# Performance work log

Measured on AMD Instinct MI355X. Metric: run time of the kernel, lower is better.

Reference implementation:

```python
import jax, jax.numpy as jnp
import numpy as np
import math

D_MODEL = 2048
NUM_HEADS = 16
HEAD_DIM = D_MODEL // NUM_HEADS
B, QLEN, CACHE_LEN = 4, 512, 3584

def setup_inputs() -> dict:
    key = jax.random.key(0)
    ks = jax.random.split(key, 13)
    s = 0.02
    return {
        'query': jax.random.normal(ks[0], (B, QLEN, D_MODEL), jnp.float32),
        'key': jax.random.normal(ks[1], (B, QLEN, D_MODEL), jnp.float32),
        'value': jax.random.normal(ks[2], (B, QLEN, D_MODEL), jnp.float32),
        'cached_k': jax.random.normal(ks[3], (B, CACHE_LEN, D_MODEL), jnp.float32),
        'cached_v': jax.random.normal(ks[4], (B, CACHE_LEN, D_MODEL), jnp.float32),
        'wq': jax.random.normal(ks[5], (D_MODEL, D_MODEL), jnp.float32) * s,
        'bq': jnp.zeros((D_MODEL,), jnp.float32),
        'wk': jax.random.normal(ks[6], (D_MODEL, D_MODEL), jnp.float32) * s,
        'bk': jnp.zeros((D_MODEL,), jnp.float32),
        'wv': jax.random.normal(ks[7], (D_MODEL, D_MODEL), jnp.float32) * s,
        'bv': jnp.zeros((D_MODEL,), jnp.float32),
        'wo': jax.random.normal(ks[8], (D_MODEL, D_MODEL), jnp.float32) * s,
        'bo': jnp.zeros((D_MODEL,), jnp.float32),
    }

def _split_heads(x):
    b, s, _ = x.shape
    return x.reshape(b, s, NUM_HEADS, HEAD_DIM).transpose(0, 2, 1, 3)  # [b,h,s,d]

def reference(query, key, value, cached_k, cached_v, wq, bq, wk, bk, wv, bv, wo, bo):
    # projections (torch Linear: x @ W^T + b)
    Q = query @ wq.T + bq
    K_new = key @ wk.T + bk
    V_new = value @ wv.T + bv
    K = jnp.concatenate([cached_k, K_new], axis=1)  # [b, total, d_model]
    V = jnp.concatenate([cached_v, V_new], axis=1)
    seq_len = query.shape[1]
    total_len = K.shape[1]
    cache_len = total_len - seq_len
    Qh = _split_heads(Q)  # [b,h,q,d]
    Kh = _split_heads(K)  # [b,h,t,d]
    Vh = _split_heads(V)
    scale = math.sqrt(HEAD_DIM)
    scores = jnp.einsum('bhqd,bhtd->bhqt', Qh, Kh) / scale
    # causal mask with cache offset: query i attends to keys j <= cache_len + i
    q_idx = jnp.arange(seq_len)[:, None]
    k_idx = jnp.arange(total_len)[None, :]
    mask = k_idx > (q_idx + cache_len)  # True = masked
    scores = jnp.where(mask[None, None], -jnp.inf, scores)
    attn = jax.nn.softmax(scores, axis=-1)
    out = jnp.einsum('bhqt,bhtd->bhqd', attn, Vh)
    out = out.transpose(0, 2, 1, 3).reshape(query.shape[0], seq_len, D_MODEL)
    out = out @ wo.T + bo
    return out
```

## Files before the change

kernel.cpp:

```cpp
#include <hip/hip_runtime.h>

typedef _Float16 half8 __attribute__((ext_vector_type(8)));
typedef _Float16 half4v __attribute__((ext_vector_type(4)));
typedef float f32x4 __attribute__((ext_vector_type(4)));

#define NB 4
#define SQ 512
#define CL 3584
#define TT 4096
#define DM 2048
#define NH 16
#define DH 128

#define KSW(row, col) ((((row) * 128) + (col)) ^ ((((row) & 7) << 3)))
#define VSW(row, col) ((((row) * 64) + (col)) ^ ((((row) & 7) << 3)))
#define PSW(row, col) ((((row) * 64) + (col)) ^ ((((row) & 7) << 3)))

__device__ __forceinline__ void gl_lds16(const void* g, void* l) {
  __builtin_amdgcn_global_load_lds(
      (const __attribute__((address_space(1))) unsigned int*)g,
      (__attribute__((address_space(3))) unsigned int*)l, 16, 0, 0);
}

__global__ __launch_bounds__(256) void cvt_f16(
    const float* __restrict__ s0, const float* __restrict__ s1, const float* __restrict__ s2,
    const float* __restrict__ s3, const float* __restrict__ s4, const float* __restrict__ s5,
    _Float16* __restrict__ d0, _Float16* __restrict__ d1, _Float16* __restrict__ d2,
    _Float16* __restrict__ d3, _Float16* __restrict__ d4, _Float16* __restrict__ d5)
{
  const int z = blockIdx.y;
  const float* s = z == 0 ? s0 : z == 1 ? s1 : z == 2 ? s2 : z == 3 ? s3 : z == 4 ? s4 : s5;
  _Float16* d = z == 0 ? d0 : z == 1 ? d1 : z == 2 ? d2 : z == 3 ? d3 : z == 4 ? d4 : d5;
  const int dstride = z < 3 ? 4096 : 2048;
  const int n4 = DM * DM / 4;
  for (int v = blockIdx.x * blockDim.x + threadIdx.x; v < n4;
       v += gridDim.x * blockDim.x) {
    float4 x = ((const float4*)s)[v];
    half4v h = { (_Float16)x.x, (_Float16)x.y, (_Float16)x.z, (_Float16)x.w };
    const int m = v >> 9, c = (v << 2) & 2047;
    *(half4v*)&d[(size_t)m * dstride + c] = h;
  }
}

__global__ __launch_bounds__(256) void cvt_f16_one(
    const float* __restrict__ s, _Float16* __restrict__ d)
{
  const int n4 = DM * DM / 4;
  for (int v = blockIdx.x * blockDim.x + threadIdx.x; v < n4;
       v += gridDim.x * blockDim.x) {
    float4 x = ((const float4*)s)[v];
    half4v h = { (_Float16)x.x, (_Float16)x.y, (_Float16)x.z, (_Float16)x.w };
    ((half4v*)d)[v] = h;
  }
}

__global__ __launch_bounds__(256) void convert_K(
    const float* __restrict__ ck, _Float16* __restrict__ K)
{
  const long long nvec = (long long)NB * CL * DM / 4;
  const int pb = CL * DM / 4;
  for (long long v = (long long)blockIdx.x * blockDim.x + threadIdx.x; v < nvec;
       v += (long long)gridDim.x * blockDim.x) {
    int b = (int)(v / pb);
    long long r = v - (long long)b * pb;
    float4 x = ((const float4*)ck)[v];
    half4v hx = { (_Float16)x.x, (_Float16)x.y, (_Float16)x.z, (_Float16)x.w };
    ((half4v*)K)[(long long)b * (TT * DM / 4) + r] = hx;
  }
}

__global__ __launch_bounds__(256) void transpose_V(
    const float* __restrict__ cv, _Float16* __restrict__ Vt)
{
  __shared__ _Float16 T[64][72];
  const int t0 = blockIdx.x * 64;
  const int dm0 = blockIdx.y * 64;
  const int b = blockIdx.z;
  const int tid = threadIdx.x;
  {
    const int tr = tid >> 2, c0 = (tid & 3) * 16;
    const float* src = cv + ((size_t)b * CL + t0 + tr) * DM + dm0 + c0;
    float4 a0 = ((const float4*)src)[0];
    float4 a1 = ((const float4*)src)[1];
    float4 a2 = ((const float4*)src)[2];
    float4 a3 = ((const float4*)src)[3];
    half8 h0 = { (_Float16)a0.x, (_Float16)a0.y, (_Float16)a0.z, (_Float16)a0.w,
                 (_Float16)a1.x, (_Float16)a1.y, (_Float16)a1.z, (_Float16)a1.w };
    half8 h1 = { (_Float16)a2.x, (_Float16)a2.y, (_Float16)a2.z, (_Float16)a2.w,
                 (_Float16)a3.x, (_Float16)a3.y, (_Float16)a3.z, (_Float16)a3.w };
    *(half8*)&T[tr][c0] = h0;
    *(half8*)&T[tr][c0 + 8] = h1;
  }
  __syncthreads();
  {
    const int dl = tid >> 2, tc = (tid & 3) * 16;
    const int h = dm0 >> 7, d = (dm0 & 127) + dl;
    half8 o0, o1;
#pragma unroll
    for (int i = 0; i < 8; ++i) o0[i] = T[tc + i][dl];
#pragma unroll
    for (int i = 0; i < 8; ++i) o1[i] = T[tc + 8 + i][dl];
    _Float16* dst = Vt + ((size_t)(b * NH + h) * DH + d) * TT + t0 + tc;
    *(half8*)dst = o0;
    *(half8*)(dst + 8) = o1;
  }
}

template<int MODE>
__global__ __launch_bounds__(512, 4) void mm16(
    const _Float16* __restrict__ A0, const _Float16* __restrict__ A1,
    const _Float16* __restrict__ A2, int astride,
    const _Float16* __restrict__ W0, const _Float16* __restrict__ W1,
    const _Float16* __restrict__ W2,
    const float* __restrict__ b0, const float* __restrict__ b1,
    const float* __restrict__ b2,
    _Float16* __restrict__ Qp, _Float16* __restrict__ Kc,
    _Float16* __restrict__ Vt, float* __restrict__ Co)
{
  __shared__ __align__(16) char smem[4 * 8192];
  char* Abuf = smem;
  char* Wbuf = smem + 2 * 8192;

  const int tid = threadIdx.x;
  const int bm = blockIdx.x, bn = blockIdx.y, z = blockIdx.z;
  const _Float16* Ain = z == 0 ? A0 : z == 1 ? A1 : A2;
  const _Float16* W   = z == 0 ? W0 : z == 1 ? W1 : W2;
  const float* bias   = z == 0 ? b0 : z == 1 ? b1 : b2;

  const int wid = tid >> 6, lane = tid & 63;
  const int wm = wid >> 2, wn = wid & 3;
  const int lr = lane & 15, lg = lane >> 4;

  f32x4 acc[4][2];
#pragma unroll
  for (int i = 0; i < 4; ++i)
#pragma unroll
    for (int j = 0; j < 2; ++j) acc[i][j] = (f32x4){0.f, 0.f, 0.f, 0.f};

  size_t aoff, woff;
  {
    const int o = wid * 1024 + lane * 16;
    const int prow = o >> 7, pb = o & 127;
    const int lb = pb ^ ((prow & 7) << 4);
    const int r = (prow << 1) | (lb >> 6), c = lb & 63;
    aoff = (size_t)(bm * 128 + r) * astride + c;
    woff = (size_t)(bn * 128 + r) * 4096 + c;
  }

  auto stage = [&](int kt, int buf) {
    gl_lds16((const char*)Ain + aoff + kt * 64, Abuf + buf * 8192 + wid * 1024);
    gl_lds16((const char*)W + woff + kt * 64, Wbuf + buf * 8192 + wid * 1024);
  };

  auto lds_addr = [](const char* base, int r, int cb) -> const char* {
    return base + ((r >> 1) << 7) + ((((r & 1) << 6) | cb) ^ (((r >> 1) & 7) << 4));
  };

  auto compute = [&](int buf) {
    const char* ab = Abuf + buf * 8192;
    const char* wb = Wbuf + buf * 8192;
    half8 af[4], bf[2];
#pragma unroll
    for (int i = 0; i < 4; ++i)
      af[i] = *(const half8*)lds_addr(ab, wm * 64 + i * 16 + lr, lg << 4);
#pragma unroll
    for (int j = 0; j < 2; ++j)
      bf[j] = *(const half8*)lds_addr(wb, wn * 32 + j * 16 + lr, lg << 4);
#pragma unroll
    for (int i = 0; i < 4; ++i)
#pragma unroll
      for (int j = 0; j < 2; ++j)
        acc[i][j] = __builtin_amdgcn_mfma_f32_16x16x32_f16(af[i], bf[j], acc[i][j], 0, 0, 0);
  };

  const int NKT = DM / 32;
  stage(0, 0);
  __syncthreads();
  for (int kt = 0; kt < NKT; ++kt) {
    if (kt + 1 < NKT) stage(kt + 1, (kt + 1) & 1);
    compute(kt & 1);
    __syncthreads();
  }

  const float qscale = 0.08838834764831845f * 1.4426950408889634f;
#pragma unroll
  for (int i = 0; i < 4; ++i) {
    const int m0 = bm * 128 + wm * 64 + i * 16 + lg * 4;
#pragma unroll
    for (int j = 0; j < 2; ++j) {
      const int gn = bn * 128 + wn * 32 + j * 16 + lr;
      const float bb = bias[gn];
      if constexpr (MODE == 1) {
#pragma unroll
        for (int r = 0; r < 4; ++r)
          Co[(size_t)(m0 + r) * DM + gn] = acc[i][j][r] + bb;
      } else {
        if (z == 0) {
#pragma unroll
          for (int r = 0; r < 4; ++r)
            Qp[(size_t)(m0 + r) * DM + gn] = (_Float16)((acc[i][j][r] + bb) * qscale);
        } else if (z == 1) {
          const int b = m0 >> 9;
#pragma unroll
          for (int r = 0; r < 4; ++r)
            Kc[((size_t)b * TT + CL + ((m0 + r) & 511)) * DM + gn] =
                (_Float16)(acc[i][j][r] + bb);
        } else {
          half4v hv;
#pragma unroll
          for (int r = 0; r < 4; ++r) hv[r] = (_Float16)(acc[i][j][r] + bb);
          const int b = m0 >> 9, t = CL + (m0 & 511);
          const int h = gn >> 7, d = gn & 127;
          *(half4v*)&Vt[((size_t)(b * NH + h) * DH + d) * TT + t] = hv;
        }
      }
    }
  }
}

__global__ __launch_bounds__(512) void attn_kernel(
    const _Float16* __restrict__ Qp, const _Float16* __restrict__ Kc,
    const _Float16* __restrict__ Vt, _Float16* __restrict__ O0,
    _Float16* __restrict__ O1, float2* __restrict__ ml)
{
  __shared__ _Float16 Ks[2][64 * 128];
  __shared__ _Float16 VTs[3][128 * 64];
  __shared__ _Float16 Ps[8][32 * 64];

  const int tid = threadIdx.x;
  const int lin = blockIdx.x;
  const int xcd = lin & 7, slot = lin >> 3;
  const int pair = xcd * 8 + (slot >> 2);
  const int rem = slot & 3;
  const int qb = rem >> 1, part = rem & 1;
  const int b = pair >> 4, h = pair & 15;

  const int wid = tid >> 6, lane = tid & 63;
  const int lr = lane & 15, lg = lane >> 4;
  const int qw = qb * 256 + wid * 32;

  half8 qf[2][4];
#pragma unroll
  for (int qs = 0; qs < 2; ++qs)
#pragma unroll
    for (int kk = 0; kk < 4; ++kk)
      qf[qs][kk] = *(const half8*)&Qp[(size_t)(b * SQ + qw + qs * 16 + lr) * DM +
                                      h * DH + kk * 32 + lg * 8];

  f32x4 zero = {0.f, 0.f, 0.f, 0.f};
  f32x4 acc[8][2];
#pragma unroll
  for (int d = 0; d < 8; ++d)
#pragma unroll
    for (int qs = 0; qs < 2; ++qs) acc[d][qs] = zero;
  float m_run[2] = {-1e30f, -1e30f}, l_run[2] = {0.f, 0.f};

  const int nt_full = (CL + qb * 256 + 256) / 64;
  const int halfn = nt_full >> 1;
  const int tbeg = part ? halfn : 0;
  const int nt = part ? (nt_full - halfn) : halfn;

  int ksrc[2], vsrc[2];
#pragma unroll
  for (int c = 0; c < 2; ++c) {
    const int p = c * 512 + wid * 64 + lane;
    { const int r = p >> 4, pg = p & 15, gc = pg ^ (r & 7);
      ksrc[c] = r * DM + gc * 8; }
    { const int d = p >> 3, pg = p & 7, gt = pg ^ (d & 7);
      vsrc[c] = d * TT + gt * 8; }
  }
  const _Float16* Kb = Kc + (size_t)b * TT * DM + h * DH;
  const _Float16* Vb = Vt + (size_t)(b * NH + h) * DH * TT;

  auto stage = [&](int tt, int kbuf, int vbuf) {
    const int t0 = (tbeg + tt) * 64;
#pragma unroll
    for (int c = 0; c < 2; ++c)
      gl_lds16(Kb + (size_t)t0 * DM + ksrc[c], &Ks[kbuf][(c * 512 + wid * 64) * 8]);
#pragma unroll
    for (int c = 0; c < 2; ++c)
      gl_lds16(Vb + t0 + vsrc[c], &VTs[vbuf][(c * 512 + wid * 64) * 8]);
  };

  auto qk = [&](int kbuf, f32x4 (*s)[2]) {
#pragma unroll
    for (int j = 0; j < 4; ++j)
#pragma unroll
      for (int qs = 0; qs < 2; ++qs) s[j][qs] = zero;
    __builtin_amdgcn_s_setprio(1);
#pragma unroll
    for (int kk = 0; kk < 4; ++kk)
#pragma unroll
      for (int j = 0; j < 4; ++j) {
        half8 kb = *(const half8*)&Ks[kbuf][KSW(j * 16 + lr, kk * 32 + lg * 8)];
        s[j][0] = __builtin_amdgcn_mfma_f32_16x16x32_f16(kb, qf[0][kk], s[j][0], 0, 0, 0);
        s[j][1] = __builtin_amdgcn_mfma_f32_16x16x32_f16(kb, qf[1][kk], s[j][1], 0, 0, 0);
      }
    __builtin_amdgcn_s_setprio(0);
  };

  auto mask_s = [&](int t0, f32x4 (*s)[2]) {
    if (part && t0 + 63 > CL + qw) {
#pragma unroll
      for (int j = 0; j < 4; ++j)
#pragma unroll
        for (int qs = 0; qs < 2; ++qs)
#pragma unroll
          for (int r = 0; r < 4; ++r)
            if (t0 + j * 16 + lg * 4 + r > CL + qw + qs * 16 + lr) s[j][qs][r] = -1e30f;
    }
  };

  auto softmax_step = [&](f32x4 (*s)[2]) {
    float mt[2];
#pragma unroll
    for (int qs = 0; qs < 2; ++qs) {
      float m = s[0][qs][0];
#pragma unroll
      for (int j = 0; j < 4; ++j)
#pragma unroll
        for (int r = 0; r < 4; ++r) m = fmaxf(m, s[j][qs][r]);
      mt[qs] = m;
    }
    if (!__all(mt[0] <= m_run[0] + 10.0f && mt[1] <= m_run[1] + 10.0f)) {
#pragma unroll
      for (int qs = 0; qs < 2; ++qs) {
        float m = fmaxf(mt[qs], __shfl_xor(mt[qs], 16));
        m = fmaxf(m, __shfl_xor(m, 32));
        const float mn = fmaxf(m_run[qs], m);
        const float fsc = exp2f(m_run[qs] - mn);
        m_run[qs] = mn;
        l_run[qs] *= fsc;
#pragma unroll
        for (int d = 0; d < 8; ++d)
#pragma unroll
          for (int r = 0; r < 4; ++r) acc[d][qs][r] *= fsc;
      }
    }
#pragma unroll
    for (int qs = 0; qs < 2; ++qs) {
      float ps = 0.f;
#pragma unroll
      for (int j = 0; j < 4; ++j) {
        float p0 = exp2f(s[j][qs][0] - m_run[qs]);
        float p1 = exp2f(s[j][qs][1] - m_run[qs]);
        float p2 = exp2f(s[j][qs][2] - m_run[qs]);
        float p3 = exp2f(s[j][qs][3] - m_run[qs]);
        ps += (p0 + p1) + (p2 + p3);
        half4v hp = { (_Float16)p0, (_Float16)p1, (_Float16)p2, (_Float16)p3 };
        *(half4v*)&Ps[wid][PSW(qs * 16 + lr, j * 16 + lg * 4)] = hp;
      }
      l_run[qs] += ps;
    }
  };

  auto pv = [&](int vbuf) {
    __builtin_amdgcn_s_setprio(1);
#pragma unroll
    for (int kk = 0; kk < 2; ++kk) {
      half8 pf0 = *(const half8*)&Ps[wid][PSW(lr, kk * 32 + lg * 8)];
      half8 pf1 = *(const half8*)&Ps[wid][PSW(16 + lr, kk * 32 + lg * 8)];
#pragma unroll
      for (int d = 0; d < 8; ++d) {
        half8 vf = *(const half8*)&VTs[vbuf][VSW(d * 16 + lr, kk * 32 + lg * 8)];
        acc[d][0] = __builtin_amdgcn_mfma_f32_16x16x32_f16(vf, pf0, acc[d][0], 0, 0, 0);
        acc[d][1] = __builtin_amdgcn_mfma_f32_16x16x32_f16(vf, pf1, acc[d][1], 0, 0, 0);
      }
    }
    __builtin_amdgcn_s_setprio(0);
  };

  f32x4 sp[4][2], sc[4][2];

  stage(0, 0, 0);
  __syncthreads();
  stage(1, 1, 1);
  qk(0, sp);
  mask_s(tbeg * 64, sp);

  for (int t = 1; t < nt; ++t) {
    __syncthreads();
    if (t + 1 < nt) stage(t + 1, (t + 1) & 1, (t + 1) % 3);
    qk(t & 1, sc);
    softmax_step(sp);
    pv((t - 1) % 3);
    mask_s((tbeg + t) * 64, sc);
#pragma unroll
    for (int j = 0; j < 4; ++j)
#pragma unroll
      for (int qs = 0; qs < 2; ++qs) sp[j][qs] = sc[j][qs];
  }
  softmax_step(sp);
  pv((nt - 1) % 3);

  _Float16* Od = part ? O1 : O0;
#pragma unroll
  for (int qs = 0; qs < 2; ++qs) {
    float lt = l_run[qs] + __shfl_xor(l_run[qs], 16);
    lt += __shfl_xor(lt, 32);
    const float inv = 1.0f / lt;
#pragma unroll
    for (int d = 0; d < 8; ++d) {
      half4v hv;
#pragma unroll
      for (int r = 0; r < 4; ++r) hv[r] = (_Float16)(acc[d][qs][r] * inv);
      *(half4v*)&Od[(size_t)(b * SQ + qw + qs * 16 + lr) * DM + h * DH + d * 16 + lg * 4] = hv;
    }
    if (lg == 0) {
      float2 e; e.x = m_run[qs]; e.y = lt;
      ml[part * (64 * SQ) + ((b * NH + h) * SQ) + qw + qs * 16 + lr] = e;
    }
  }
}

__global__ __launch_bounds__(256) void combine(
    _Float16* __restrict__ AO, const _Float16* __restrict__ O1,
    const float2* __restrict__ ml)
{
  const int idx = blockIdx.x * 256 + threadIdx.x;
  const int row = idx >> 8;
  const int col0 = (idx & 255) * 8;
  const int b = row >> 9, q = row & 511, h = col0 >> 7;
  const float2 e0 = ml[(b * NH + h) * SQ + q];
  const float2 e1 = ml[64 * SQ + (b * NH + h) * SQ + q];
  const float m = fmaxf(e0.x, e1.x);
  float w0 = e0.y * exp2f(e0.x - m);
  float w1 = e1.y * exp2f(e1.x - m);
  const float inv = 1.0f / (w0 + w1);
  w0 *= inv; w1 *= inv;
  const size_t o = (size_t)row * DM + col0;
  half8 a = *(const half8*)&AO[o];
  half8 c = *(const half8*)&O1[o];
  half8 r;
#pragma unroll
  for (int i = 0; i < 8; ++i)
    r[i] = (_Float16)(w0 * (float)a[i] + w1 * (float)c[i]);
  *(half8*)&AO[o] = r;
}

extern "C" void kernel_launch(void* const* d_in, const int* in_sizes, int n_in,
                              void* d_out, int out_size, void* d_ws, size_t ws_size,
                              hipStream_t stream) {
  const float* query = (const float*)d_in[0];
  const float* key   = (const float*)d_in[1];
  const float* value = (const float*)d_in[2];
  const float* ck    = (const float*)d_in[3];
  const float* cv    = (const float*)d_in[4];
  const float* wq = (const float*)d_in[5];
  const float* bq = (const float*)d_in[6];
  const float* wk = (const float*)d_in[7];
  const float* bk = (const float*)d_in[8];
  const float* wv = (const float*)d_in[9];
  const float* bv = (const float*)d_in[10];
  const float* wo = (const float*)d_in[11];
  const float* bo = (const float*)d_in[12];

  char* ws = (char*)d_ws;
  _Float16* Kc = (_Float16*)ws;
  _Float16* Vt = (_Float16*)(ws + 67108864);
  _Float16* Qp = (_Float16*)(ws + 134217728);
  _Float16* AO = (_Float16*)(ws + 142606336);

  _Float16* O1s = (_Float16*)d_out;
  float2* mls = (float2*)((char*)d_out + 8388608);

  _Float16* wqh = Kc;
  _Float16* wkh = Kc + 8388608;
  _Float16* wvh = Kc + 16777216;
  _Float16* qh = Vt;
  _Float16* kh = Vt + 2048 * 4096;
  _Float16* vh = Vt + 4096 * 4096;
  _Float16* woh = Qp;

  cvt_f16<<<dim3(512, 6), 256, 0, stream>>>(
      query, key, value, wq, wk, wv, qh, kh, vh, wqh, wkh, wvh);
  mm16<0><<<dim3(16, 16, 3), 512, 0, stream>>>(
      qh, kh, vh, 8192, wqh, wkh, wvh, bq, bk, bv, Qp, Kc, Vt, nullptr);
  convert_K<<<2048, 256, 0, stream>>>(ck, Kc);
  transpose_V<<<dim3(CL / 64, DM / 64, NB), 256, 0, stream>>>(cv, Vt);
  attn_kernel<<<256, 512, 0, stream>>>(Qp, Kc, Vt, AO, O1s, mls);
  combine<<<2048, 256, 0, stream>>>(AO, O1s, mls);
  cvt_f16_one<<<512, 256, 0, stream>>>(wo, woh);
  mm16<1><<<dim3(16, 16, 1), 512, 0, stream>>>(
      AO, AO, AO, 4096, woh, woh, woh, bo, bo, bo, nullptr, nullptr, nullptr,
      (float*)d_out);
}
```

Baseline: 323.0 us.

## Fuse QKV projection GEMM with cached-V transpose into one launch

```diff
diff --git a/kernel.cpp b/kernel.cpp
--- a/kernel.cpp
+++ b/kernel.cpp
@@ -31,14 +31,12 @@
   const int z = blockIdx.y;
   const float* s = z == 0 ? s0 : z == 1 ? s1 : z == 2 ? s2 : z == 3 ? s3 : z == 4 ? s4 : s5;
   _Float16* d = z == 0 ? d0 : z == 1 ? d1 : z == 2 ? d2 : z == 3 ? d3 : z == 4 ? d4 : d5;
-  const int dstride = z < 3 ? 4096 : 2048;
   const int n4 = DM * DM / 4;
   for (int v = blockIdx.x * blockDim.x + threadIdx.x; v < n4;
        v += gridDim.x * blockDim.x) {
     float4 x = ((const float4*)s)[v];
     half4v h = { (_Float16)x.x, (_Float16)x.y, (_Float16)x.z, (_Float16)x.w };
-    const int m = v >> 9, c = (v << 2) & 2047;
-    *(half4v*)&d[(size_t)m * dstride + c] = h;
+    ((half4v*)d)[v] = h;
   }
 }
 
@@ -69,64 +67,157 @@
   }
 }
 
-__global__ __launch_bounds__(256) void transpose_V(
-    const float* __restrict__ cv, _Float16* __restrict__ Vt)
-{
-  __shared__ _Float16 T[64][72];
-  const int t0 = blockIdx.x * 64;
-  const int dm0 = blockIdx.y * 64;
-  const int b = blockIdx.z;
-  const int tid = threadIdx.x;
-  {
-    const int tr = tid >> 2, c0 = (tid & 3) * 16;
-    const float* src = cv + ((size_t)b * CL + t0 + tr) * DM + dm0 + c0;
-    float4 a0 = ((const float4*)src)[0];
-    float4 a1 = ((const float4*)src)[1];
-    float4 a2 = ((const float4*)src)[2];
-    float4 a3 = ((const float4*)src)[3];
-    half8 h0 = { (_Float16)a0.x, (_Float16)a0.y, (_Float16)a0.z, (_Float16)a0.w,
-                 (_Float16)a1.x, (_Float16)a1.y, (_Float16)a1.z, (_Float16)a1.w };
-    half8 h1 = { (_Float16)a2.x, (_Float16)a2.y, (_Float16)a2.z, (_Float16)a2.w,
-                 (_Float16)a3.x, (_Float16)a3.y, (_Float16)a3.z, (_Float16)a3.w };
-    *(half8*)&T[tr][c0] = h0;
-    *(half8*)&T[tr][c0 + 8] = h1;
-  }
-  __syncthreads();
-  {
-    const int dl = tid >> 2, tc = (tid & 3) * 16;
-    const int h = dm0 >> 7, d = (dm0 & 127) + dl;
-    half8 o0, o1;
-#pragma unroll
-    for (int i = 0; i < 8; ++i) o0[i] = T[tc + i][dl];
-#pragma unroll
-    for (int i = 0; i < 8; ++i) o1[i] = T[tc + 8 + i][dl];
-    _Float16* dst = Vt + ((size_t)(b * NH + h) * DH + d) * TT + t0 + tc;
-    *(half8*)dst = o0;
-    *(half8*)(dst + 8) = o1;
-  }
-}
-
-template<int MODE>
-__global__ __launch_bounds__(512, 4) void mm16(
+__global__ __launch_bounds__(512) void fused_pre(
     const _Float16* __restrict__ A0, const _Float16* __restrict__ A1,
-    const _Float16* __restrict__ A2, int astride,
+    const _Float16* __restrict__ A2,
     const _Float16* __restrict__ W0, const _Float16* __restrict__ W1,
     const _Float16* __restrict__ W2,
     const float* __restrict__ b0, const float* __restrict__ b1,
     const float* __restrict__ b2,
     _Float16* __restrict__ Qp, _Float16* __restrict__ Kc,
-    _Float16* __restrict__ Vt, float* __restrict__ Co)
+    _Float16* __restrict__ Vt, const float* __restrict__ cv)
+{
+  __shared__ __align__(16) char smem[4 * 8192];
+
+  const int bid = blockIdx.x;
+  const int tid = threadIdx.x;
+
+  if (bid < 768) {
+    char* Abuf = smem;
+    char* Wbuf = smem + 2 * 8192;
+    const int bm = bid & 15, bn = (bid >> 4) & 15, z = bid >> 8;
+    const _Float16* Ain = z == 0 ? A0 : z == 1 ? A1 : A2;
+    const _Float16* W   = z == 0 ? W0 : z == 1 ? W1 : W2;
+    const float* bias   = z == 0 ? b0 : z == 1 ? b1 : b2;
+
+    const int wid = tid >> 6, lane = tid & 63;
+    const int wm = wid >> 2, wn = wid & 3;
+    const int lr = lane & 15, lg = lane >> 4;
+
+    f32x4 acc[4][2];
+#pragma unroll
+    for (int i = 0; i < 4; ++i)
+#pragma unroll
+      for (int j = 0; j < 2; ++j) acc[i][j] = (f32x4){0.f, 0.f, 0.f, 0.f};
+
+    size_t aoff, woff;
+    {
+      const int o = wid * 1024 + lane * 16;
+      const int prow = o >> 7, pb = o & 127;
+      const int lb = pb ^ ((prow & 7) << 4);
+      const int r = (prow << 1) | (lb >> 6), c = lb & 63;
+      aoff = (size_t)(bm * 128 + r) * 4096 + c;
+      woff = (size_t)(bn * 128 + r) * 4096 + c;
+    }
+
+    auto stage = [&](int kt, int buf) {
+      gl_lds16((const char*)Ain + aoff + kt * 64, Abuf + buf * 8192 + wid * 1024);
+      gl_lds16((const char*)W + woff + kt * 64, Wbuf + buf * 8192 + wid * 1024);
+    };
+    auto lds_addr = [](const char* base, int r, int cb) -> const char* {
+      return base + ((r >> 1) << 7) + ((((r & 1) << 6) | cb) ^ (((r >> 1) & 7) << 4));
+    };
+    auto compute = [&](int buf) {
+      const char* ab = Abuf + buf * 8192;
+      const char* wb = Wbuf + buf * 8192;
+      half8 af[4], bf[2];
+#pragma unroll
+      for (int i = 0; i < 4; ++i)
+        af[i] = *(const half8*)lds_addr(ab, wm * 64 + i * 16 + lr, lg << 4);
+#pragma unroll
+      for (int j = 0; j < 2; ++j)
+        bf[j] = *(const half8*)lds_addr(wb, wn * 32 + j * 16 + lr, lg << 4);
+#pragma unroll
+      for (int i = 0; i < 4; ++i)
+#pragma unroll
+        for (int j = 0; j < 2; ++j)
+          acc[i][j] = __builtin_amdgcn_mfma_f32_16x16x32_f16(af[i], bf[j], acc[i][j], 0, 0, 0);
+    };
+
+    const int NKT = DM / 32;
+    stage(0, 0);
+    __syncthreads();
+    for (int kt = 0; kt < NKT; ++kt) {
+      if (kt + 1 < NKT) stage(kt + 1, (kt + 1) & 1);
+      compute(kt & 1);
+      __syncthreads();
+    }
+
+    const float qscale = 0.08838834764831845f * 1.4426950408889634f;
+#pragma unroll
+    for (int i = 0; i < 4; ++i) {
+      const int m0 = bm * 128 + wm * 64 + i * 16 + lg * 4;
+#pragma unroll
+      for (int j = 0; j < 2; ++j) {
+        const int gn = bn * 128 + wn * 32 + j * 16 + lr;
+        const float bb = bias[gn];
+        if (z == 0) {
+#pragma unroll
+          for (int r = 0; r < 4; ++r)
+            Qp[(size_t)(m0 + r) * DM + gn] = (_Float16)((acc[i][j][r] + bb) * qscale);
+        } else if (z == 1) {
+          const int b = m0 >> 9;
+#pragma unroll
+          for (int r = 0; r < 4; ++r)
+            Kc[((size_t)b * TT + CL + ((m0 + r) & 511)) * DM + gn] =
+                (_Float16)(acc[i][j][r] + bb);
+        } else {
+          half4v hv;
+#pragma unroll
+          for (int r = 0; r < 4; ++r) hv[r] = (_Float16)(acc[i][j][r] + bb);
+          const int b = m0 >> 9, t = CL + (m0 & 511);
+          const int h = gn >> 7, d = gn & 127;
+          *(half4v*)&Vt[((size_t)(b * NH + h) * DH + d) * TT + t] = hv;
+        }
+      }
+    }
+  } else {
+    _Float16 (*T)[136] = (_Float16(*)[136])smem;
+    const int tv = bid - 768;
+    const int b = tv / 896;
+    const int rem = tv - b * 896;
+    const int t0 = (rem % 56) * 64;
+    const int dm0 = (rem / 56) * 128;
+    {
+      const int tr = tid >> 3, c0 = (tid & 7) * 16;
+      const float* src = cv + ((size_t)b * CL + t0 + tr) * DM + dm0 + c0;
+      float4 a0 = ((const float4*)src)[0];
+      float4 a1 = ((const float4*)src)[1];
+      float4 a2 = ((const float4*)src)[2];
+      float4 a3 = ((const float4*)src)[3];
+      half8 h0 = { (_Float16)a0.x, (_Float16)a0.y, (_Float16)a0.z, (_Float16)a0.w,
+                   (_Float16)a1.x, (_Float16)a1.y, (_Float16)a1.z, (_Float16)a1.w };
+      half8 h1 = { (_Float16)a2.x, (_Float16)a2.y, (_Float16)a2.z, (_Float16)a2.w,
+                   (_Float16)a3.x, (_Float16)a3.y, (_Float16)a3.z, (_Float16)a3.w };
+      *(half8*)&T[tr][c0] = h0;
+      *(half8*)&T[tr][c0 + 8] = h1;
+    }
+    __syncthreads();
+    {
+      const int dl = tid >> 2, tc = (tid & 3) * 16;
+      const int h = dm0 >> 7;
+      half8 o0, o1;
+#pragma unroll
+      for (int i = 0; i < 8; ++i) o0[i] = T[tc + i][dl];
+#pragma unroll
+      for (int i = 0; i < 8; ++i) o1[i] = T[tc + 8 + i][dl];
+      _Float16* dst = Vt + ((size_t)(b * NH + h) * DH + dl) * TT + t0 + tc;
+      *(half8*)dst = o0;
+      *(half8*)(dst + 8) = o1;
+    }
+  }
+}
+
+__global__ __launch_bounds__(512, 4) void mm16o(
+    const _Float16* __restrict__ Ain, const _Float16* __restrict__ W,
+    const float* __restrict__ bias, float* __restrict__ Co)
 {
   __shared__ __align__(16) char smem[4 * 8192];
   char* Abuf = smem;
   char* Wbuf = smem + 2 * 8192;
 
   const int tid = threadIdx.x;
-  const int bm = blockIdx.x, bn = blockIdx.y, z = blockIdx.z;
-  const _Float16* Ain = z == 0 ? A0 : z == 1 ? A1 : A2;
-  const _Float16* W   = z == 0 ? W0 : z == 1 ? W1 : W2;
-  const float* bias   = z == 0 ? b0 : z == 1 ? b1 : b2;
-
+  const int bm = blockIdx.x, bn = blockIdx.y;
   const int wid = tid >> 6, lane = tid & 63;
   const int wm = wid >> 2, wn = wid & 3;
   const int lr = lane & 15, lg = lane >> 4;
@@ -143,7 +234,7 @@
     const int prow = o >> 7, pb = o & 127;
     const int lb = pb ^ ((prow & 7) << 4);
     const int r = (prow << 1) | (lb >> 6), c = lb & 63;
-    aoff = (size_t)(bm * 128 + r) * astride + c;
+    aoff = (size_t)(bm * 128 + r) * 4096 + c;
     woff = (size_t)(bn * 128 + r) * 4096 + c;
   }
 
@@ -151,11 +242,9 @@
     gl_lds16((const char*)Ain + aoff + kt * 64, Abuf + buf * 8192 + wid * 1024);
     gl_lds16((const char*)W + woff + kt * 64, Wbuf + buf * 8192 + wid * 1024);
   };
-
   auto lds_addr = [](const char* base, int r, int cb) -> const char* {
     return base + ((r >> 1) << 7) + ((((r & 1) << 6) | cb) ^ (((r >> 1) & 7) << 4));
   };
-
   auto compute = [&](int buf) {
     const char* ab = Abuf + buf * 8192;
     const char* wb = Wbuf + buf * 8192;
@@ -182,7 +271,6 @@
     __syncthreads();
   }
 
-  const float qscale = 0.08838834764831845f * 1.4426950408889634f;
 #pragma unroll
   for (int i = 0; i < 4; ++i) {
     const int m0 = bm * 128 + wm * 64 + i * 16 + lg * 4;
@@ -190,30 +278,9 @@
     for (int j = 0; j < 2; ++j) {
       const int gn = bn * 128 + wn * 32 + j * 16 + lr;
       const float bb = bias[gn];
-      if constexpr (MODE == 1) {
-#pragma unroll
-        for (int r = 0; r < 4; ++r)
-          Co[(size_t)(m0 + r) * DM + gn] = acc[i][j][r] + bb;
-      } else {
-        if (z == 0) {
-#pragma unroll
-          for (int r = 0; r < 4; ++r)
-            Qp[(size_t)(m0 + r) * DM + gn] = (_Float16)((acc[i][j][r] + bb) * qscale);
-        } else if (z == 1) {
-          const int b = m0 >> 9;
-#pragma unroll
-          for (int r = 0; r < 4; ++r)
-            Kc[((size_t)b * TT + CL + ((m0 + r) & 511)) * DM + gn] =
-                (_Float16)(acc[i][j][r] + bb);
-        } else {
-          half4v hv;
-#pragma unroll
-          for (int r = 0; r < 4; ++r) hv[r] = (_Float16)(acc[i][j][r] + bb);
-          const int b = m0 >> 9, t = CL + (m0 & 511);
-          const int h = gn >> 7, d = gn & 127;
-          *(half4v*)&Vt[((size_t)(b * NH + h) * DH + d) * TT + t] = hv;
-        }
-      }
+#pragma unroll
+      for (int r = 0; r < 4; ++r)
+        Co[(size_t)(m0 + r) * DM + gn] = acc[i][j][r] + bb;
     }
   }
 }
@@ -287,7 +354,6 @@
     for (int j = 0; j < 4; ++j)
 #pragma unroll
       for (int qs = 0; qs < 2; ++qs) s[j][qs] = zero;
-    __builtin_amdgcn_s_setprio(1);
 #pragma unroll
     for (int kk = 0; kk < 4; ++kk)
 #pragma unroll
@@ -296,7 +362,6 @@
         s[j][0] = __builtin_amdgcn_mfma_f32_16x16x32_f16(kb, qf[0][kk], s[j][0], 0, 0, 0);
         s[j][1] = __builtin_amdgcn_mfma_f32_16x16x32_f16(kb, qf[1][kk], s[j][1], 0, 0, 0);
       }
-    __builtin_amdgcn_s_setprio(0);
   };
 
   auto mask_s = [&](int t0, f32x4 (*s)[2]) {
@@ -355,7 +420,6 @@
   };
 
   auto pv = [&](int vbuf) {
-    __builtin_amdgcn_s_setprio(1);
 #pragma unroll
     for (int kk = 0; kk < 2; ++kk) {
       half8 pf0 = *(const half8*)&Ps[wid][PSW(lr, kk * 32 + lg * 8)];
@@ -367,7 +431,6 @@
         acc[d][1] = __builtin_amdgcn_mfma_f32_16x16x32_f16(vf, pf1, acc[d][1], 0, 0, 0);
       }
     }
-    __builtin_amdgcn_s_setprio(0);
   };
 
   f32x4 sp[4][2], sc[4][2];
@@ -461,27 +524,24 @@
   _Float16* Qp = (_Float16*)(ws + 134217728);
   _Float16* AO = (_Float16*)(ws + 142606336);
 
+  _Float16* qh = AO;
+  _Float16* kh = (_Float16*)d_out;
+  _Float16* vh = (_Float16*)((char*)d_out + 8388608);
+  _Float16* wqh = Kc;
+  _Float16* wkh = (_Float16*)(ws + 16777216);
+  _Float16* wvh = (_Float16*)(ws + 33554432);
+  _Float16* woh = Qp;
+
   _Float16* O1s = (_Float16*)d_out;
   float2* mls = (float2*)((char*)d_out + 8388608);
 
-  _Float16* wqh = Kc;
-  _Float16* wkh = Kc + 8388608;
-  _Float16* wvh = Kc + 16777216;
-  _Float16* qh = Vt;
-  _Float16* kh = Vt + 2048 * 4096;
-  _Float16* vh = Vt + 4096 * 4096;
-  _Float16* woh = Qp;
-
   cvt_f16<<<dim3(512, 6), 256, 0, stream>>>(
       query, key, value, wq, wk, wv, qh, kh, vh, wqh, wkh, wvh);
-  mm16<0><<<dim3(16, 16, 3), 512, 0, stream>>>(
-      qh, kh, vh, 8192, wqh, wkh, wvh, bq, bk, bv, Qp, Kc, Vt, nullptr);
+  fused_pre<<<768 + 3584, 512, 0, stream>>>(
+      qh, kh, vh, wqh, wkh, wvh, bq, bk, bv, Qp, Kc, Vt, cv);
   convert_K<<<2048, 256, 0, stream>>>(ck, Kc);
-  transpose_V<<<dim3(CL / 64, DM / 64, NB), 256, 0, stream>>>(cv, Vt);
   attn_kernel<<<256, 512, 0, stream>>>(Qp, Kc, Vt, AO, O1s, mls);
   combine<<<2048, 256, 0, stream>>>(AO, O1s, mls);
   cvt_f16_one<<<512, 256, 0, stream>>>(wo, woh);
-  mm16<1><<<dim3(16, 16, 1), 512, 0, stream>>>(
-      AO, AO, AO, 4096, woh, woh, woh, bo, bo, bo, nullptr, nullptr, nullptr,
-      (float*)d_out);
-}
+  mm16o<<<dim3(16, 16), 512, 0, stream>>>(AO, woh, bo, (float*)d_out);
+}
```

After: 315.7 us. 1.02x faster.
